# Kernel optimization log

Hardware: AMD Instinct MI355X
Metric: run time of the kernel (lower is better)

The kernel has to match this reference:

```python
import jax, jax.numpy as jnp
import numpy as np

N, F_IN, F_OUT = 20000, 512, 512
E = 320000
S = 6           # max_subgraph_size
T = 0.5         # evolution_time
HSCALE = 0.05   # Hamiltonian scale
MAX_TERMS = 4   # truncated matrix-exp series terms
EPS = 1e-5      # BatchNorm eps


def _build_subgraphs(edge_index_np):
    # deterministic stand-in for SubgraphCache: 1-hop in-neighbors, center first,
    # truncated to S nodes (matches mapping=0 after subsampling in the original)
    loops = np.stack([np.arange(N), np.arange(N)])
    ei = np.concatenate([edge_index_np.astype(np.int64), loops], axis=1)
    codes = np.unique(ei[0] * N + ei[1])   # dedup directed edges incl. self loops
    src, dst = codes // N, codes % N
    order = np.argsort(dst, kind='stable')
    src_s, dst_s = src[order], dst[order]
    starts = np.searchsorted(dst_s, np.arange(N))
    ends = np.searchsorted(dst_s, np.arange(N) + 1)
    sub_nodes = np.zeros((N, S), dtype=np.int32)
    valid = np.zeros((N, S), dtype=bool)
    for i in range(N):
        nb = np.unique(src_s[starts[i]:ends[i]])
        nb = nb[nb != i][:S - 1]
        k = 1 + nb.shape[0]
        sub_nodes[i, 0] = i
        sub_nodes[i, 1:k] = nb
        valid[i, :k] = True
    # induced directed adjacency of each size-S subgraph (padded slots zeroed)
    pair = sub_nodes[:, :, None].astype(np.int64) * N + sub_nodes[:, None, :].astype(np.int64)
    hit = np.isin(pair, codes)
    pv = valid[:, :, None] & valid[:, None, :]
    sub_adj = (hit & pv).astype(np.int32)
    return jnp.asarray(sub_nodes), jnp.asarray(sub_adj)


def setup_inputs() -> dict:
    key = jax.random.key(0)
    ks = jax.random.split(key, 4)
    x = jax.random.normal(ks[0], (N, F_IN), dtype=jnp.float32)
    edge_index = jax.random.randint(ks[1], (2, E), 0, N, dtype=jnp.int32)
    sub_nodes, sub_adj = _build_subgraphs(np.asarray(edge_index))
    W_re = jax.random.normal(ks[2], (F_IN, F_OUT), dtype=jnp.float32) * 0.02
    W_im = jax.random.normal(ks[3], (F_IN, F_OUT), dtype=jnp.float32) * 0.02
    b_re = jnp.zeros((F_OUT,), jnp.float32)
    b_im = jnp.zeros((F_OUT,), jnp.float32)
    gamma_r = jnp.ones((F_OUT,), jnp.float32)
    beta_r = jnp.zeros((F_OUT,), jnp.float32)
    gamma_i = jnp.ones((F_OUT,), jnp.float32)
    beta_i = jnp.zeros((F_OUT,), jnp.float32)
    return {"x": x, "edge_index": edge_index, "sub_nodes": sub_nodes,
            "sub_adj": sub_adj, "W_re": W_re, "W_im": W_im, "b_re": b_re,
            "b_im": b_im, "gamma_r": gamma_r, "beta_r": beta_r,
            "gamma_i": gamma_i, "beta_i": beta_i}


def _bn(v, gamma, beta):
    # training-mode BatchNorm1d (biased variance), applied per real/imag part
    mu = v.mean(axis=0)
    var = jnp.var(v, axis=0)
    return (v - mu) * jax.lax.rsqrt(var + EPS) * gamma + beta


def reference(x, edge_index, sub_nodes, sub_adj, W_re, W_im, b_re, b_im,
              gamma_r, beta_r, gamma_i, beta_i):
    # ComplexLinear on real-valued input: y = x @ (W_re + i W_im) + b
    y = jax.lax.complex(x @ W_re + b_re, x @ W_im + b_im)    # [N, F_OUT] c64
    # per-node subgraph Laplacian Hamiltonian: L = diag(deg) - A, H = 0.05 * L
    A = sub_adj.astype(jnp.float32)                          # [N, S, S]
    deg = A.sum(-1)                                          # degree(row)
    L = deg[:, :, None] * jnp.eye(S, dtype=jnp.float32) - A
    scaled = (-1j * T * HSCALE) * L.astype(jnp.complex64)    # -i * H * t
    # center row (index 0) of truncated series exp(-iHt); lower block of the
    # 2dim unitary hits zero-padded z rows, so only U_sub row 0 matters
    v = jnp.zeros((N, S), jnp.complex64).at[:, 0].set(1.0)
    term, res = v, v
    for k in range(1, MAX_TERMS + 1):
        term = jnp.einsum('ns,nst->nt', term, scaled) / k
        res = res + term
    sub_x = y[sub_nodes]                                     # [N, S, F_OUT]
    evolved = jnp.einsum('ns,nsf->nf', res, sub_x)           # center of U @ z
    # complex ReLU -> naive complex BatchNorm -> residual (in==out, no proj)
    er, ei = jax.nn.relu(evolved.real), jax.nn.relu(evolved.imag)
    out_r = _bn(er, gamma_r, beta_r) + x
    out_i = _bn(ei, gamma_i, beta_i)
    # complex output represented as concat(real, imag)
    return jnp.concatenate([out_r, out_i], axis=-1)          # [N, 2*F_OUT]
```

## Files before the change

### kernel.cpp

```cpp
#include <hip/hip_runtime.h>

#define N_NODES 20000
#define FDIM 512
#define SSZ 6

typedef __attribute__((ext_vector_type(8))) short bf16x8;
typedef __attribute__((ext_vector_type(4))) float f32x4;
typedef __attribute__((ext_vector_type(8))) unsigned short u16x8;

static __device__ __forceinline__ unsigned short f2bf(float f) {
    unsigned int u = __float_as_uint(f);
    unsigned int r = (u + 0x7fffu + ((u >> 16) & 1u)) >> 16;
    return (unsigned short)r;
}
static __device__ __forceinline__ float bf2f(unsigned short u) {
    return __uint_as_float(((unsigned int)u) << 16);
}

__global__ __launch_bounds__(256) void conv_x(
    const float* __restrict__ x, unsigned short* __restrict__ xb)
{
    const size_t i = ((size_t)blockIdx.x * 256 + threadIdx.x) * 8;
    const float4 a = *(const float4*)(x + i);
    const float4 b = *(const float4*)(x + i + 4);
    u16x8 o;
    o[0] = f2bf(a.x); o[1] = f2bf(a.y); o[2] = f2bf(a.z); o[3] = f2bf(a.w);
    o[4] = f2bf(b.x); o[5] = f2bf(b.y); o[6] = f2bf(b.z); o[7] = f2bf(b.w);
    *(u16x8*)(xb + i) = o;
}

__global__ __launch_bounds__(256) void conv_wt(
    const float* __restrict__ Wre, const float* __restrict__ Wim,
    unsigned short* __restrict__ wt)
{
    __shared__ float tile[32][33];
    const float* W = blockIdx.z ? Wim : Wre;
    const int tx = threadIdx.x, ty = threadIdx.y;
    const int k0 = blockIdx.x * 32;
    const int n0 = blockIdx.y * 32;
#pragma unroll
    for (int i = 0; i < 4; ++i)
        tile[ty + i * 8][tx] = W[(size_t)(k0 + ty + i * 8) * FDIM + n0 + tx];
    __syncthreads();
    unsigned short* wtb = wt + (size_t)blockIdx.z * FDIM * FDIM;
#pragma unroll
    for (int i = 0; i < 4; ++i)
        wtb[(size_t)(n0 + ty + i * 8) * FDIM + k0 + tx] = f2bf(tile[tx][ty + i * 8]);
}

#define BM 128
#define BN 128
#define BK 64

__global__ __launch_bounds__(256) void gemm_mfma(
    const unsigned short* __restrict__ xb,
    const unsigned short* __restrict__ wt,
    const float* __restrict__ bre, const float* __restrict__ bim,
    unsigned short* __restrict__ y)
{
    __shared__ __align__(16) unsigned short lA[BM * BK];
    __shared__ __align__(16) unsigned short lB[BN * BK];

    const int tid  = threadIdx.x;
    const int wave = tid >> 6;
    const int lane = tid & 63;
    const int rowBase = blockIdx.y * BM;
    const int colBase = blockIdx.x * BN;

    const int wm = (wave >> 1) * 64;
    const int wn = (wave & 1) * 64;

    f32x4 acc[4][4];
#pragma unroll
    for (int i = 0; i < 4; ++i)
#pragma unroll
        for (int j = 0; j < 4; ++j) acc[i][j] = (f32x4){0.f, 0.f, 0.f, 0.f};

    const int srow   = lane >> 3;
    const int schunk = lane & 7;
    const int gchunk = schunk ^ srow;
    const int aRow0  = wave * 32;

    const int fm = lane & 15;
    const int kq = lane >> 4;

    for (int k0 = 0; k0 < FDIM; k0 += BK) {
#pragma unroll
        for (int i = 0; i < 4; ++i) {
            const int trow = aRow0 + i * 8;
            int grow = rowBase + trow + srow;
            if (grow > N_NODES - 1) grow = N_NODES - 1;
            const unsigned short* gp = xb + (size_t)grow * FDIM + k0 + gchunk * 8;
            __builtin_amdgcn_global_load_lds(
                (const __attribute__((address_space(1))) void*)gp,
                (__attribute__((address_space(3))) void*)(lA + trow * BK), 16, 0, 0);
        }
#pragma unroll
        for (int i = 0; i < 4; ++i) {
            const int trow = aRow0 + i * 8;
            const int grow = colBase + trow + srow;
            const unsigned short* gp = wt + (size_t)grow * FDIM + k0 + gchunk * 8;
            __builtin_amdgcn_global_load_lds(
                (const __attribute__((address_space(1))) void*)gp,
                (__attribute__((address_space(3))) void*)(lB + trow * BK), 16, 0, 0);
        }
        __syncthreads();

#pragma unroll
        for (int ks = 0; ks < 2; ++ks) {
            bf16x8 af[4], bfr[4];
            const int g = ks * 4 + kq;
#pragma unroll
            for (int mt = 0; mt < 4; ++mt) {
                const int row = wm + mt * 16 + fm;
                af[mt] = *(const bf16x8*)&lA[row * BK + ((g ^ (row & 7)) << 3)];
            }
#pragma unroll
            for (int nt = 0; nt < 4; ++nt) {
                const int row = wn + nt * 16 + fm;
                bfr[nt] = *(const bf16x8*)&lB[row * BK + ((g ^ (row & 7)) << 3)];
            }
#pragma unroll
            for (int mt = 0; mt < 4; ++mt)
#pragma unroll
                for (int nt = 0; nt < 4; ++nt)
                    acc[mt][nt] = __builtin_amdgcn_mfma_f32_16x16x32_bf16(
                        af[mt], bfr[nt], acc[mt][nt], 0, 0, 0);
        }
        __syncthreads();
    }

    const int rquad = lane >> 4;
#pragma unroll
    for (int nt = 0; nt < 4; ++nt) {
        const int col = colBase + wn + nt * 16 + fm;
        const float bias = (col < FDIM) ? bre[col] : bim[col - FDIM];
#pragma unroll
        for (int mt = 0; mt < 4; ++mt) {
            const int row0 = rowBase + wm + mt * 16 + rquad * 4;
#pragma unroll
            for (int r = 0; r < 4; ++r) {
                const int row = row0 + r;
                if (row < N_NODES)
                    y[(size_t)row * 1024 + col] = f2bf(acc[mt][nt][r] + bias);
            }
        }
    }
}

__global__ __launch_bounds__(256) void evolve_relu(
    const unsigned short* __restrict__ y,
    const int* __restrict__ sub_nodes,
    const int* __restrict__ sub_adj,
    unsigned short* __restrict__ eb)
{
    const int wave = threadIdx.x >> 6;
    const int lane = threadIdx.x & 63;
    const int n = blockIdx.x * 4 + wave;

    const int* sa = sub_adj + (size_t)n * (SSZ * SSZ);
    float A[SSZ][SSZ], deg[SSZ];
#pragma unroll
    for (int s = 0; s < SSZ; ++s) {
        float d = 0.f;
#pragma unroll
        for (int t = 0; t < SSZ; ++t) { float a = (float)sa[s * SSZ + t]; A[s][t] = a; d += a; }
        deg[s] = d;
    }
    float p1[SSZ], p2[SSZ], p3[SSZ], p4[SSZ];
#pragma unroll
    for (int t = 0; t < SSZ; ++t) p1[t] = ((t == 0) ? deg[0] : 0.f) - A[0][t];
#pragma unroll
    for (int t = 0; t < SSZ; ++t) {
        float acc = 0.f;
#pragma unroll
        for (int s = 0; s < SSZ; ++s) acc += p1[s] * (((s == t) ? deg[s] : 0.f) - A[s][t]);
        p2[t] = acc;
    }
#pragma unroll
    for (int t = 0; t < SSZ; ++t) {
        float acc = 0.f;
#pragma unroll
        for (int s = 0; s < SSZ; ++s) acc += p2[s] * (((s == t) ? deg[s] : 0.f) - A[s][t]);
        p3[t] = acc;
    }
#pragma unroll
    for (int t = 0; t < SSZ; ++t) {
        float acc = 0.f;
#pragma unroll
        for (int s = 0; s < SSZ; ++s) acc += p3[s] * (((s == t) ? deg[s] : 0.f) - A[s][t]);
        p4[t] = acc;
    }
    float rre[SSZ], rim[SSZ];
#pragma unroll
    for (int t = 0; t < SSZ; ++t) {
        rre[t] = ((t == 0) ? 1.f : 0.f) - 3.125e-4f * p2[t] + 1.6276041666666668e-8f * p4[t];
        rim[t] = -0.025f * p1[t] + 2.6041666666666666e-6f * p3[t];
    }

    const int f = lane << 3;
    float aR[8] = {0.f}, aI[8] = {0.f};
#pragma unroll
    for (int s = 0; s < SSZ; ++s) {
        const int nd = sub_nodes[n * SSZ + s];
        const float cr = rre[s], ci = rim[s];
        const unsigned short* base = y + (size_t)nd * 1024 + f;
        const u16x8 yr8 = *(const u16x8*)base;
        const u16x8 yi8 = *(const u16x8*)(base + FDIM);
#pragma unroll
        for (int j = 0; j < 8; ++j) {
            const float yr = bf2f(yr8[j]);
            const float yi = bf2f(yi8[j]);
            aR[j] = fmaf(cr, yr, fmaf(-ci, yi, aR[j]));
            aI[j] = fmaf(cr, yi, fmaf(ci, yr, aI[j]));
        }
    }
    u16x8 er8, ei8;
#pragma unroll
    for (int j = 0; j < 8; ++j) {
        er8[j] = f2bf(fmaxf(aR[j], 0.f));
        ei8[j] = f2bf(fmaxf(aI[j], 0.f));
    }
    *(u16x8*)(eb + (size_t)n * 1024 + f) = er8;
    *(u16x8*)(eb + (size_t)n * 1024 + FDIM + f) = ei8;
}

__global__ __launch_bounds__(512) void stats_kernel(
    const unsigned short* __restrict__ eb, float* __restrict__ sums)
{
    const int tid = threadIdx.x;
    const int r0 = blockIdx.x * 40;
    float sr = 0.f, sr2 = 0.f, si = 0.f, si2 = 0.f;
    for (int r = r0; r < r0 + 40; ++r) {
        const float vr = bf2f(eb[(size_t)r * 1024 + tid]);
        const float vi = bf2f(eb[(size_t)r * 1024 + FDIM + tid]);
        sr += vr; sr2 = fmaf(vr, vr, sr2);
        si += vi; si2 = fmaf(vi, vi, si2);
    }
    atomicAdd(&sums[tid], sr);
    atomicAdd(&sums[512 + tid], sr2);
    atomicAdd(&sums[1024 + tid], si);
    atomicAdd(&sums[1536 + tid], si2);
}

__global__ __launch_bounds__(512) void bnparams_kernel(
    const float* __restrict__ sums,
    const float* __restrict__ gr, const float* __restrict__ br_,
    const float* __restrict__ gi, const float* __restrict__ bi_,
    float* __restrict__ prm)
{
    const int f = threadIdx.x;
    const float invN = 1.0f / (float)N_NODES;
    const float mur = sums[f] * invN;
    const float varr = fmaf(-mur, mur, sums[512 + f] * invN);
    const float scr = rsqrtf(varr + 1e-5f) * gr[f];
    prm[f] = scr;
    prm[512 + f] = fmaf(-mur, scr, br_[f]);
    const float mui = sums[1024 + f] * invN;
    const float vari = fmaf(-mui, mui, sums[1536 + f] * invN);
    const float sci = rsqrtf(vari + 1e-5f) * gi[f];
    prm[1024 + f] = sci;
    prm[1536 + f] = fmaf(-mui, sci, bi_[f]);
}

__global__ __launch_bounds__(256) void finalize_kernel(
    const float* __restrict__ x, const unsigned short* __restrict__ eb,
    const float* __restrict__ prm, float* __restrict__ out)
{
    const int gid = blockIdx.x * 256 + threadIdx.x;
    const int n = gid >> 6;
    const int f = (gid & 63) << 3;
    const u16x8 er8 = *(const u16x8*)(eb + (size_t)n * 1024 + f);
    const u16x8 ei8 = *(const u16x8*)(eb + (size_t)n * 1024 + FDIM + f);
    float orr[8], oii[8];
#pragma unroll
    for (int j = 0; j < 8; ++j) {
        const float scr = prm[f + j],        shr = prm[512 + f + j];
        const float sci = prm[1024 + f + j], shi = prm[1536 + f + j];
        const float xv = x[(size_t)n * FDIM + f + j];
        orr[j] = fmaf(bf2f(er8[j]), scr, shr) + xv;
        oii[j] = fmaf(bf2f(ei8[j]), sci, shi);
    }
#pragma unroll
    for (int j = 0; j < 8; j += 4) {
        *(float4*)(out + (size_t)n * 1024 + f + j) =
            make_float4(orr[j], orr[j + 1], orr[j + 2], orr[j + 3]);
        *(float4*)(out + (size_t)n * 1024 + FDIM + f + j) =
            make_float4(oii[j], oii[j + 1], oii[j + 2], oii[j + 3]);
    }
}

extern "C" void kernel_launch(void* const* d_in, const int* in_sizes, int n_in,
                              void* d_out, int out_size, void* d_ws, size_t ws_size,
                              hipStream_t stream)
{
    const float* x        = (const float*)d_in[0];
    const int* sub_nodes  = (const int*)d_in[2];
    const int* sub_adj    = (const int*)d_in[3];
    const float* Wre      = (const float*)d_in[4];
    const float* Wim      = (const float*)d_in[5];
    const float* bre      = (const float*)d_in[6];
    const float* bim      = (const float*)d_in[7];
    const float* gr       = (const float*)d_in[8];
    const float* br_      = (const float*)d_in[9];
    const float* gi       = (const float*)d_in[10];
    const float* bi_      = (const float*)d_in[11];
    float* out = (float*)d_out;

    unsigned short* y  = (unsigned short*)d_ws;
    unsigned short* eb = y + (size_t)N_NODES * 1024;
    unsigned short* xb = eb + (size_t)N_NODES * 1024;
    unsigned short* wt = xb + (size_t)N_NODES * FDIM;
    float* sums        = (float*)(wt + (size_t)1024 * FDIM);
    float* prm         = sums + 2048;

    hipMemsetAsync(sums, 0, 2048 * sizeof(float), stream);

    conv_x<<<(N_NODES * FDIM) / (256 * 8), 256, 0, stream>>>(x, xb);
    conv_wt<<<dim3(16, 16, 2), dim3(32, 8), 0, stream>>>(Wre, Wim, wt);

    dim3 gg(1024 / BN, (N_NODES + BM - 1) / BM);
    gemm_mfma<<<gg, 256, 0, stream>>>(xb, wt, bre, bim, y);

    evolve_relu<<<N_NODES / 4, 256, 0, stream>>>(y, sub_nodes, sub_adj, eb);
    stats_kernel<<<500, 512, 0, stream>>>(eb, sums);
    bnparams_kernel<<<1, 512, 0, stream>>>(sums, gr, br_, gi, bi_, prm);
    finalize_kernel<<<(N_NODES * 64) / 256, 256, 0, stream>>>(x, eb, prm, out);
}
```

Before: 266.2 us.

## Fuse conversion kernels and memset, fold BN stats into evolve, shrink GEMM tile

Result: faster. 248.8 us (-6.5%).

```diff
diff --git a/kernel.cpp b/kernel.cpp
--- a/kernel.cpp
+++ b/kernel.cpp
@@ -17,38 +17,45 @@
     return __uint_as_float(((unsigned int)u) << 16);
 }
 
-__global__ __launch_bounds__(256) void conv_x(
-    const float* __restrict__ x, unsigned short* __restrict__ xb)
-{
-    const size_t i = ((size_t)blockIdx.x * 256 + threadIdx.x) * 8;
-    const float4 a = *(const float4*)(x + i);
-    const float4 b = *(const float4*)(x + i + 4);
-    u16x8 o;
-    o[0] = f2bf(a.x); o[1] = f2bf(a.y); o[2] = f2bf(a.z); o[3] = f2bf(a.w);
-    o[4] = f2bf(b.x); o[5] = f2bf(b.y); o[6] = f2bf(b.z); o[7] = f2bf(b.w);
-    *(u16x8*)(xb + i) = o;
-}
-
-__global__ __launch_bounds__(256) void conv_wt(
-    const float* __restrict__ Wre, const float* __restrict__ Wim,
-    unsigned short* __restrict__ wt)
-{
-    __shared__ float tile[32][33];
-    const float* W = blockIdx.z ? Wim : Wre;
-    const int tx = threadIdx.x, ty = threadIdx.y;
-    const int k0 = blockIdx.x * 32;
-    const int n0 = blockIdx.y * 32;
-#pragma unroll
-    for (int i = 0; i < 4; ++i)
-        tile[ty + i * 8][tx] = W[(size_t)(k0 + ty + i * 8) * FDIM + n0 + tx];
-    __syncthreads();
-    unsigned short* wtb = wt + (size_t)blockIdx.z * FDIM * FDIM;
-#pragma unroll
-    for (int i = 0; i < 4; ++i)
-        wtb[(size_t)(n0 + ty + i * 8) * FDIM + k0 + tx] = f2bf(tile[tx][ty + i * 8]);
-}
-
-#define BM 128
+__global__ __launch_bounds__(256) void conv_all(
+    const float* __restrict__ x, const float* __restrict__ Wre,
+    const float* __restrict__ Wim, unsigned short* __restrict__ xb,
+    unsigned short* __restrict__ wt, float* __restrict__ sums)
+{
+    const int blk = blockIdx.x;
+    const int tid = threadIdx.x;
+    if (blk < 5000) {
+        const size_t i = ((size_t)blk * 256 + tid) * 8;
+        const float4 a = *(const float4*)(x + i);
+        const float4 b = *(const float4*)(x + i + 4);
+        u16x8 o;
+        o[0] = f2bf(a.x); o[1] = f2bf(a.y); o[2] = f2bf(a.z); o[3] = f2bf(a.w);
+        o[4] = f2bf(b.x); o[5] = f2bf(b.y); o[6] = f2bf(b.z); o[7] = f2bf(b.w);
+        *(u16x8*)(xb + i) = o;
+    } else if (blk < 5512) {
+        __shared__ float tile[32][33];
+        const int bidx = blk - 5000;
+        const int z = bidx >> 8;
+        const int rem = bidx & 255;
+        const int k0 = (rem & 15) * 32;
+        const int n0 = (rem >> 4) * 32;
+        const float* W = z ? Wim : Wre;
+        const int tx = tid & 31, ty = tid >> 5;
+#pragma unroll
+        for (int i = 0; i < 4; ++i)
+            tile[ty + i * 8][tx] = W[(size_t)(k0 + ty + i * 8) * FDIM + n0 + tx];
+        __syncthreads();
+        unsigned short* wtb = wt + (size_t)z * FDIM * FDIM;
+#pragma unroll
+        for (int i = 0; i < 4; ++i)
+            wtb[(size_t)(n0 + ty + i * 8) * FDIM + k0 + tx] = f2bf(tile[tx][ty + i * 8]);
+    } else {
+#pragma unroll
+        for (int i = 0; i < 8; ++i) sums[i * 256 + tid] = 0.f;
+    }
+}
+
+#define BM 64
 #define BN 128
 #define BK 64
 
@@ -67,27 +74,26 @@
     const int rowBase = blockIdx.y * BM;
     const int colBase = blockIdx.x * BN;
 
-    const int wm = (wave >> 1) * 64;
+    const int wm = (wave >> 1) * 32;
     const int wn = (wave & 1) * 64;
 
-    f32x4 acc[4][4];
-#pragma unroll
-    for (int i = 0; i < 4; ++i)
+    f32x4 acc[2][4];
+#pragma unroll
+    for (int i = 0; i < 2; ++i)
 #pragma unroll
         for (int j = 0; j < 4; ++j) acc[i][j] = (f32x4){0.f, 0.f, 0.f, 0.f};
 
     const int srow   = lane >> 3;
     const int schunk = lane & 7;
     const int gchunk = schunk ^ srow;
-    const int aRow0  = wave * 32;
 
     const int fm = lane & 15;
     const int kq = lane >> 4;
 
     for (int k0 = 0; k0 < FDIM; k0 += BK) {
 #pragma unroll
-        for (int i = 0; i < 4; ++i) {
-            const int trow = aRow0 + i * 8;
+        for (int i = 0; i < 2; ++i) {
+            const int trow = wave * 16 + i * 8;
             int grow = rowBase + trow + srow;
             if (grow > N_NODES - 1) grow = N_NODES - 1;
             const unsigned short* gp = xb + (size_t)grow * FDIM + k0 + gchunk * 8;
@@ -97,7 +103,7 @@
         }
 #pragma unroll
         for (int i = 0; i < 4; ++i) {
-            const int trow = aRow0 + i * 8;
+            const int trow = wave * 32 + i * 8;
             const int grow = colBase + trow + srow;
             const unsigned short* gp = wt + (size_t)grow * FDIM + k0 + gchunk * 8;
             __builtin_amdgcn_global_load_lds(
@@ -108,10 +114,10 @@
 
 #pragma unroll
         for (int ks = 0; ks < 2; ++ks) {
-            bf16x8 af[4], bfr[4];
+            bf16x8 af[2], bfr[4];
             const int g = ks * 4 + kq;
 #pragma unroll
-            for (int mt = 0; mt < 4; ++mt) {
+            for (int mt = 0; mt < 2; ++mt) {
                 const int row = wm + mt * 16 + fm;
                 af[mt] = *(const bf16x8*)&lA[row * BK + ((g ^ (row & 7)) << 3)];
             }
@@ -121,7 +127,7 @@
                 bfr[nt] = *(const bf16x8*)&lB[row * BK + ((g ^ (row & 7)) << 3)];
             }
 #pragma unroll
-            for (int mt = 0; mt < 4; ++mt)
+            for (int mt = 0; mt < 2; ++mt)
 #pragma unroll
                 for (int nt = 0; nt < 4; ++nt)
                     acc[mt][nt] = __builtin_amdgcn_mfma_f32_16x16x32_bf16(
@@ -136,7 +142,7 @@
         const int col = colBase + wn + nt * 16 + fm;
         const float bias = (col < FDIM) ? bre[col] : bim[col - FDIM];
 #pragma unroll
-        for (int mt = 0; mt < 4; ++mt) {
+        for (int mt = 0; mt < 2; ++mt) {
             const int row0 = rowBase + wm + mt * 16 + rquad * 4;
 #pragma unroll
             for (int r = 0; r < 4; ++r) {
@@ -148,138 +154,171 @@
     }
 }
 
-__global__ __launch_bounds__(256) void evolve_relu(
+__global__ __launch_bounds__(256) void evolve_stats(
     const unsigned short* __restrict__ y,
     const int* __restrict__ sub_nodes,
     const int* __restrict__ sub_adj,
-    unsigned short* __restrict__ eb)
-{
+    unsigned short* __restrict__ eb,
+    float* __restrict__ sums)
+{
+    __shared__ float lsum[2048];
     const int wave = threadIdx.x >> 6;
     const int lane = threadIdx.x & 63;
-    const int n = blockIdx.x * 4 + wave;
-
-    const int* sa = sub_adj + (size_t)n * (SSZ * SSZ);
-    float A[SSZ][SSZ], deg[SSZ];
-#pragma unroll
-    for (int s = 0; s < SSZ; ++s) {
-        float d = 0.f;
-#pragma unroll
-        for (int t = 0; t < SSZ; ++t) { float a = (float)sa[s * SSZ + t]; A[s][t] = a; d += a; }
-        deg[s] = d;
-    }
-    float p1[SSZ], p2[SSZ], p3[SSZ], p4[SSZ];
-#pragma unroll
-    for (int t = 0; t < SSZ; ++t) p1[t] = ((t == 0) ? deg[0] : 0.f) - A[0][t];
-#pragma unroll
-    for (int t = 0; t < SSZ; ++t) {
-        float acc = 0.f;
-#pragma unroll
-        for (int s = 0; s < SSZ; ++s) acc += p1[s] * (((s == t) ? deg[s] : 0.f) - A[s][t]);
-        p2[t] = acc;
-    }
-#pragma unroll
-    for (int t = 0; t < SSZ; ++t) {
-        float acc = 0.f;
-#pragma unroll
-        for (int s = 0; s < SSZ; ++s) acc += p2[s] * (((s == t) ? deg[s] : 0.f) - A[s][t]);
-        p3[t] = acc;
-    }
-#pragma unroll
-    for (int t = 0; t < SSZ; ++t) {
-        float acc = 0.f;
-#pragma unroll
-        for (int s = 0; s < SSZ; ++s) acc += p3[s] * (((s == t) ? deg[s] : 0.f) - A[s][t]);
-        p4[t] = acc;
-    }
-    float rre[SSZ], rim[SSZ];
-#pragma unroll
-    for (int t = 0; t < SSZ; ++t) {
-        rre[t] = ((t == 0) ? 1.f : 0.f) - 3.125e-4f * p2[t] + 1.6276041666666668e-8f * p4[t];
-        rim[t] = -0.025f * p1[t] + 2.6041666666666666e-6f * p3[t];
-    }
-
     const int f = lane << 3;
-    float aR[8] = {0.f}, aI[8] = {0.f};
-#pragma unroll
-    for (int s = 0; s < SSZ; ++s) {
-        const int nd = sub_nodes[n * SSZ + s];
-        const float cr = rre[s], ci = rim[s];
-        const unsigned short* base = y + (size_t)nd * 1024 + f;
-        const u16x8 yr8 = *(const u16x8*)base;
-        const u16x8 yi8 = *(const u16x8*)(base + FDIM);
+
+    float sR[8] = {0.f}, sR2[8] = {0.f}, sI[8] = {0.f}, sI2[8] = {0.f};
+
+    for (int q = 0; q < 4; ++q) {
+        const int n = blockIdx.x * 16 + wave * 4 + q;
+
+        const int* sa = sub_adj + (size_t)n * (SSZ * SSZ);
+        float A[SSZ][SSZ], deg[SSZ];
+#pragma unroll
+        for (int s = 0; s < SSZ; ++s) {
+            float d = 0.f;
+#pragma unroll
+            for (int t = 0; t < SSZ; ++t) { float a = (float)sa[s * SSZ + t]; A[s][t] = a; d += a; }
+            deg[s] = d;
+        }
+        float p1[SSZ], p2[SSZ], p3[SSZ], p4[SSZ];
+#pragma unroll
+        for (int t = 0; t < SSZ; ++t) p1[t] = ((t == 0) ? deg[0] : 0.f) - A[0][t];
+#pragma unroll
+        for (int t = 0; t < SSZ; ++t) {
+            float acc = 0.f;
+#pragma unroll
+            for (int s = 0; s < SSZ; ++s) acc += p1[s] * (((s == t) ? deg[s] : 0.f) - A[s][t]);
+            p2[t] = acc;
+        }
+#pragma unroll
+        for (int t = 0; t < SSZ; ++t) {
+            float acc = 0.f;
+#pragma unroll
+            for (int s = 0; s < SSZ; ++s) acc += p2[s] * (((s == t) ? deg[s] : 0.f) - A[s][t]);
+            p3[t] = acc;
+        }
+#pragma unroll
+        for (int t = 0; t < SSZ; ++t) {
+            float acc = 0.f;
+#pragma unroll
+            for (int s = 0; s < SSZ; ++s) acc += p3[s] * (((s == t) ? deg[s] : 0.f) - A[s][t]);
+            p4[t] = acc;
+        }
+        float rre[SSZ], rim[SSZ];
+#pragma unroll
+        for (int t = 0; t < SSZ; ++t) {
+            rre[t] = ((t == 0) ? 1.f : 0.f) - 3.125e-4f * p2[t] + 1.6276041666666668e-8f * p4[t];
+            rim[t] = -0.025f * p1[t] + 2.6041666666666666e-6f * p3[t];
+        }
+
+        float aR[8] = {0.f}, aI[8] = {0.f};
+#pragma unroll
+        for (int s = 0; s < SSZ; ++s) {
+            const int nd = sub_nodes[n * SSZ + s];
+            const float cr = rre[s], ci = rim[s];
+            const unsigned short* base = y + (size_t)nd * 1024 + f;
+            const u16x8 yr8 = *(const u16x8*)base;
+            const u16x8 yi8 = *(const u16x8*)(base + FDIM);
+#pragma unroll
+            for (int j = 0; j < 8; ++j) {
+                const float yr = bf2f(yr8[j]);
+                const float yi = bf2f(yi8[j]);
+                aR[j] = fmaf(cr, yr, fmaf(-ci, yi, aR[j]));
+                aI[j] = fmaf(cr, yi, fmaf(ci, yr, aI[j]));
+            }
+        }
+        u16x8 er8, ei8;
 #pragma unroll
         for (int j = 0; j < 8; ++j) {
-            const float yr = bf2f(yr8[j]);
-            const float yi = bf2f(yi8[j]);
-            aR[j] = fmaf(cr, yr, fmaf(-ci, yi, aR[j]));
-            aI[j] = fmaf(cr, yi, fmaf(ci, yr, aI[j]));
-        }
-    }
-    u16x8 er8, ei8;
-#pragma unroll
-    for (int j = 0; j < 8; ++j) {
-        er8[j] = f2bf(fmaxf(aR[j], 0.f));
-        ei8[j] = f2bf(fmaxf(aI[j], 0.f));
-    }
-    *(u16x8*)(eb + (size_t)n * 1024 + f) = er8;
-    *(u16x8*)(eb + (size_t)n * 1024 + FDIM + f) = ei8;
-}
-
-__global__ __launch_bounds__(512) void stats_kernel(
-    const unsigned short* __restrict__ eb, float* __restrict__ sums)
-{
-    const int tid = threadIdx.x;
-    const int r0 = blockIdx.x * 40;
-    float sr = 0.f, sr2 = 0.f, si = 0.f, si2 = 0.f;
-    for (int r = r0; r < r0 + 40; ++r) {
-        const float vr = bf2f(eb[(size_t)r * 1024 + tid]);
-        const float vi = bf2f(eb[(size_t)r * 1024 + FDIM + tid]);
-        sr += vr; sr2 = fmaf(vr, vr, sr2);
-        si += vi; si2 = fmaf(vi, vi, si2);
-    }
-    atomicAdd(&sums[tid], sr);
-    atomicAdd(&sums[512 + tid], sr2);
-    atomicAdd(&sums[1024 + tid], si);
-    atomicAdd(&sums[1536 + tid], si2);
-}
-
-__global__ __launch_bounds__(512) void bnparams_kernel(
+            const unsigned short re = f2bf(fmaxf(aR[j], 0.f));
+            const unsigned short im = f2bf(fmaxf(aI[j], 0.f));
+            er8[j] = re; ei8[j] = im;
+            const float erv = bf2f(re), eiv = bf2f(im);
+            sR[j] += erv;  sR2[j] = fmaf(erv, erv, sR2[j]);
+            sI[j] += eiv;  sI2[j] = fmaf(eiv, eiv, sI2[j]);
+        }
+        *(u16x8*)(eb + (size_t)n * 1024 + f) = er8;
+        *(u16x8*)(eb + (size_t)n * 1024 + FDIM + f) = ei8;
+    }
+
+    if (wave == 0) {
+#pragma unroll
+        for (int j = 0; j < 8; ++j) {
+            lsum[f + j] = sR[j];  lsum[512 + f + j] = sR2[j];
+            lsum[1024 + f + j] = sI[j];  lsum[1536 + f + j] = sI2[j];
+        }
+    }
+    for (int w = 1; w < 4; ++w) {
+        __syncthreads();
+        if (wave == w) {
+#pragma unroll
+            for (int j = 0; j < 8; ++j) {
+                lsum[f + j] += sR[j];  lsum[512 + f + j] += sR2[j];
+                lsum[1024 + f + j] += sI[j];  lsum[1536 + f + j] += sI2[j];
+            }
+        }
+    }
+    __syncthreads();
+#pragma unroll
+    for (int i = 0; i < 8; ++i) {
+        const int idx = i * 256 + threadIdx.x;
+        atomicAdd(&sums[idx], lsum[idx]);
+    }
+}
+
+__global__ __launch_bounds__(256) void finalize_kernel(
+    const float* __restrict__ x, const unsigned short* __restrict__ eb,
     const float* __restrict__ sums,
     const float* __restrict__ gr, const float* __restrict__ br_,
     const float* __restrict__ gi, const float* __restrict__ bi_,
-    float* __restrict__ prm)
-{
-    const int f = threadIdx.x;
-    const float invN = 1.0f / (float)N_NODES;
-    const float mur = sums[f] * invN;
-    const float varr = fmaf(-mur, mur, sums[512 + f] * invN);
-    const float scr = rsqrtf(varr + 1e-5f) * gr[f];
-    prm[f] = scr;
-    prm[512 + f] = fmaf(-mur, scr, br_[f]);
-    const float mui = sums[1024 + f] * invN;
-    const float vari = fmaf(-mui, mui, sums[1536 + f] * invN);
-    const float sci = rsqrtf(vari + 1e-5f) * gi[f];
-    prm[1024 + f] = sci;
-    prm[1536 + f] = fmaf(-mui, sci, bi_[f]);
-}
-
-__global__ __launch_bounds__(256) void finalize_kernel(
-    const float* __restrict__ x, const unsigned short* __restrict__ eb,
-    const float* __restrict__ prm, float* __restrict__ out)
+    float* __restrict__ out)
 {
     const int gid = blockIdx.x * 256 + threadIdx.x;
     const int n = gid >> 6;
     const int f = (gid & 63) << 3;
+    const float invN = 1.0f / (float)N_NODES;
+
+    float scr[8], shr[8], sci[8], shi[8];
+#pragma unroll
+    for (int h = 0; h < 2; ++h) {
+        const int fo = f + h * 4;
+        const float4 s1 = *(const float4*)(sums + fo);
+        const float4 s2 = *(const float4*)(sums + 512 + fo);
+        const float4 s3 = *(const float4*)(sums + 1024 + fo);
+        const float4 s4 = *(const float4*)(sums + 1536 + fo);
+        const float4 g1 = *(const float4*)(gr + fo);
+        const float4 b1 = *(const float4*)(br_ + fo);
+        const float4 g2 = *(const float4*)(gi + fo);
+        const float4 b2 = *(const float4*)(bi_ + fo);
+        const float mu[4] = {s1.x * invN, s1.y * invN, s1.z * invN, s1.w * invN};
+        const float q2[4] = {s2.x * invN, s2.y * invN, s2.z * invN, s2.w * invN};
+        const float mi[4] = {s3.x * invN, s3.y * invN, s3.z * invN, s3.w * invN};
+        const float qi[4] = {s4.x * invN, s4.y * invN, s4.z * invN, s4.w * invN};
+        const float gg1[4] = {g1.x, g1.y, g1.z, g1.w};
+        const float bb1[4] = {b1.x, b1.y, b1.z, b1.w};
+        const float gg2[4] = {g2.x, g2.y, g2.z, g2.w};
+        const float bb2[4] = {b2.x, b2.y, b2.z, b2.w};
+#pragma unroll
+        for (int j = 0; j < 4; ++j) {
+            const float vr = fmaf(-mu[j], mu[j], q2[j]);
+            const float sc1 = rsqrtf(vr + 1e-5f) * gg1[j];
+            scr[h * 4 + j] = sc1;
+            shr[h * 4 + j] = fmaf(-mu[j], sc1, bb1[j]);
+            const float vi = fmaf(-mi[j], mi[j], qi[j]);
+            const float sc2 = rsqrtf(vi + 1e-5f) * gg2[j];
+            sci[h * 4 + j] = sc2;
+            shi[h * 4 + j] = fmaf(-mi[j], sc2, bb2[j]);
+        }
+    }
+
     const u16x8 er8 = *(const u16x8*)(eb + (size_t)n * 1024 + f);
     const u16x8 ei8 = *(const u16x8*)(eb + (size_t)n * 1024 + FDIM + f);
     float orr[8], oii[8];
 #pragma unroll
     for (int j = 0; j < 8; ++j) {
-        const float scr = prm[f + j],        shr = prm[512 + f + j];
-        const float sci = prm[1024 + f + j], shi = prm[1536 + f + j];
         const float xv = x[(size_t)n * FDIM + f + j];
-        orr[j] = fmaf(bf2f(er8[j]), scr, shr) + xv;
-        oii[j] = fmaf(bf2f(ei8[j]), sci, shi);
+        orr[j] = fmaf(bf2f(er8[j]), scr[j], shr[j]) + xv;
+        oii[j] = fmaf(bf2f(ei8[j]), sci[j], shi[j]);
     }
 #pragma unroll
     for (int j = 0; j < 8; j += 4) {
@@ -312,18 +351,14 @@
     unsigned short* xb = eb + (size_t)N_NODES * 1024;
     unsigned short* wt = xb + (size_t)N_NODES * FDIM;
     float* sums        = (float*)(wt + (size_t)1024 * FDIM);
-    float* prm         = sums + 2048;
-
-    hipMemsetAsync(sums, 0, 2048 * sizeof(float), stream);
-
-    conv_x<<<(N_NODES * FDIM) / (256 * 8), 256, 0, stream>>>(x, xb);
-    conv_wt<<<dim3(16, 16, 2), dim3(32, 8), 0, stream>>>(Wre, Wim, wt);
+
+    conv_all<<<5513, 256, 0, stream>>>(x, Wre, Wim, xb, wt, sums);
 
     dim3 gg(1024 / BN, (N_NODES + BM - 1) / BM);
     gemm_mfma<<<gg, 256, 0, stream>>>(xb, wt, bre, bim, y);
 
-    evolve_relu<<<N_NODES / 4, 256, 0, stream>>>(y, sub_nodes, sub_adj, eb);
-    stats_kernel<<<500, 512, 0, stream>>>(eb, sums);
-    bnparams_kernel<<<1, 512, 0, stream>>>(sums, gr, br_, gi, bi_, prm);
-    finalize_kernel<<<(N_NODES * 64) / 256, 256, 0, stream>>>(x, eb, prm, out);
-}
+    evolve_stats<<<N_NODES / 16, 256, 0, stream>>>(y, sub_nodes, sub_adj, eb, sums);
+
+    finalize_kernel<<<(N_NODES * 64) / 256, 256, 0, stream>>>(
+        x, eb, sums, gr, br_, gi, bi_, out);
+}
```
